# Optimization experiments

Hardware: AMD Instinct MI355X
Metric: run time of the kernel (lower is better)

Reference implementation:

```python
import jax, jax.numpy as jnp
import numpy as np

N_HEADS, N_POINTS, N_LEVELS = 8, 4, 1


def _bilinear(val, x, y):
    """Bilinear sample with zero padding. val: (H, W, D); x, y: (N,) pixel coords.
    Matches torch grid_sample / ms_deform_attn CUDA bilinear (zeros outside)."""
    H, W, _ = val.shape
    x0 = jnp.floor(x)
    y0 = jnp.floor(y)
    dx = (x - x0)[..., None]
    dy = (y - y0)[..., None]
    x0i = x0.astype(jnp.int32)
    y0i = y0.astype(jnp.int32)

    def g(yi, xi):
        inb = ((yi >= 0) & (yi < H) & (xi >= 0) & (xi < W))[..., None]
        yc = jnp.clip(yi, 0, H - 1)
        xc = jnp.clip(xi, 0, W - 1)
        return val[yc, xc] * inb

    v00 = g(y0i, x0i)
    v01 = g(y0i, x0i + 1)
    v10 = g(y0i + 1, x0i)
    v11 = g(y0i + 1, x0i + 1)
    return (v00 * (1 - dx) * (1 - dy) + v01 * dx * (1 - dy)
            + v10 * (1 - dx) * dy + v11 * dx * dy)


def setup_inputs() -> dict:
    key = jax.random.key(0)
    ks = jax.random.split(key, 10)
    V, Lq, C = 5, 4096, 256
    H, W = 128, 240
    nH, P, L = N_HEADS, N_POINTS, N_LEVELS

    query = jax.random.normal(ks[0], (V, Lq, C), jnp.float32)
    reference_points = jax.random.uniform(ks[1], (V, Lq, L, 2), jnp.float32)
    src0 = jax.random.normal(ks[2], (V, C, H, W), jnp.float32)
    camera_ray0 = jax.random.normal(ks[3], (V, H, W, 3), jnp.float32)
    input_spatial_shapes = jnp.array([[H, W]], jnp.int32)
    input_level_start_index = jnp.array([0], jnp.int32)

    # rayconv: Linear(d_model+3 -> d_model), xavier-like
    W_ray = jax.random.normal(ks[4], (C + 3, C), jnp.float32) * (2.0 / (C + 3 + C)) ** 0.5
    b_ray = jnp.zeros((C,), jnp.float32)

    # sampling_offsets: small random weight + the grid bias from _reset_parameters
    W_so = jax.random.normal(ks[5], (C, nH * L * P * 2), jnp.float32) * 0.01
    thetas = np.arange(nH, dtype=np.float64) * (2.0 * np.pi / nH)
    grid = np.stack([np.cos(thetas), np.sin(thetas)], -1)
    grid = grid / np.abs(grid).max(-1, keepdims=True)
    grid = np.tile(grid[:, None, None, :], (1, L, P, 1))  # (nH, L, P, 2)
    grid = grid * (np.arange(P) + 1)[None, None, :, None]
    b_so = jnp.asarray(grid.reshape(-1), jnp.float32)

    W_aw = jax.random.normal(ks[6], (C, nH * L * P), jnp.float32) * 0.01
    b_aw = jnp.zeros((nH * L * P,), jnp.float32)

    W_out = jax.random.normal(ks[7], (C, C), jnp.float32) * (2.0 / (2 * C)) ** 0.5
    b_out = jnp.zeros((C,), jnp.float32)

    return {"query": query, "reference_points": reference_points, "src0": src0,
            "camera_ray0": camera_ray0, "input_spatial_shapes": input_spatial_shapes,
            "input_level_start_index": input_level_start_index,
            "W_ray": W_ray, "b_ray": b_ray, "W_so": W_so, "b_so": b_so,
            "W_aw": W_aw, "b_aw": b_aw, "W_out": W_out, "b_out": b_out}


def reference(query, reference_points, src0, camera_ray0, input_spatial_shapes,
              input_level_start_index, W_ray, b_ray, W_so, b_so, W_aw, b_aw,
              W_out, b_out):
    V, Lq, C = query.shape
    _, _, H, W = src0.shape
    nH, P, L = N_HEADS, N_POINTS, N_LEVELS
    dh = C // nH

    # --- reference-point features via grid_sample (align_corners=False) ---
    g = jnp.clip(reference_points[:, :, 0, :] * 2.0 - 1.0, -1.1, 1.1)  # (V,Lq,2)
    gx = (g[..., 0] + 1.0) * (W * 0.5) - 0.5
    gy = (g[..., 1] + 1.0) * (H * 0.5) - 0.5
    src_hw = jnp.transpose(src0, (0, 2, 3, 1))  # (V,H,W,C)
    ref_feat = jax.vmap(_bilinear)(src_hw, gx, gy)  # (V,Lq,C)

    # --- value = rayconv(concat(flattened features, camera ray embeds)) ---
    src_flat = jnp.transpose(src0.reshape(V, C, H * W), (0, 2, 1))  # (V,Len_in,C)
    cam_flat = camera_ray0.reshape(V, H * W, 3)
    input_flatten = jnp.concatenate([src_flat, cam_flat], -1)  # (V,Len_in,C+3)
    value = input_flatten @ W_ray + b_ray  # (V,Len_in,C)
    # (V,nH,H,W,dh) for per-head bilinear gathering
    value_h = jnp.transpose(value.reshape(V, H, W, nH, dh), (0, 3, 1, 2, 4))

    # --- offsets & attention weights from (ref_feat + query) ---
    feat = ref_feat + query  # (V,Lq,C)  [n_levels==1 so the level dim collapses]
    so = (feat @ W_so + b_so).reshape(V, Lq, nH, L, P, 2)
    aw = jax.nn.softmax((feat @ W_aw + b_aw).reshape(V, Lq, nH, L * P), -1)
    aw = aw.reshape(V, Lq, nH, L, P)

    # normalizer = (W, H)
    norm = jnp.stack([input_spatial_shapes[0, 1],
                      input_spatial_shapes[0, 0]]).astype(query.dtype)
    loc = reference_points[:, :, None, :, None, :] + so / norm  # (V,Lq,nH,L,P,2)

    # --- multi-scale deformable gather (single level) ---
    lx = loc[:, :, :, 0, :, 0]  # (V,Lq,nH,P)
    ly = loc[:, :, :, 0, :, 1]
    x_im = jnp.transpose(lx, (0, 2, 1, 3)).reshape(V, nH, Lq * P) * W - 0.5
    y_im = jnp.transpose(ly, (0, 2, 1, 3)).reshape(V, nH, Lq * P) * H - 0.5
    sampled = jax.vmap(jax.vmap(_bilinear))(value_h, x_im, y_im)  # (V,nH,Lq*P,dh)
    sampled = sampled.reshape(V, nH, Lq, P, dh)

    out = jnp.einsum('vhqpd,vqhp->vqhd', sampled, aw[:, :, :, 0, :])
    out = out.reshape(V, Lq, C)
    return out @ W_out + b_out
```

## Files before the change

kernel.cpp:

```cpp
#include <hip/hip_runtime.h>

#define V_  5
#define LQ  4096
#define C_  256
#define H_  128
#define W_  240
#define HW_ (H_*W_)
#define NH  8
#define DH  32
#define NP  4

typedef __attribute__((ext_vector_type(8))) short bf16x8;
typedef __attribute__((ext_vector_type(4))) float f32x4;

__device__ __forceinline__ unsigned f2b(float f) {
    unsigned u = __float_as_uint(f);
    return (u + 0x7fffu + ((u >> 16) & 1u)) >> 16;
}
__device__ __forceinline__ unsigned pack2(float a, float b) {
    return f2b(a) | (f2b(b) << 16);
}

__global__ __launch_bounds__(256) void k_prep(const float* __restrict__ W_ray,
                                              const float* __restrict__ W_out,
                                              const float* __restrict__ W_so,
                                              const float* __restrict__ W_aw,
                                              unsigned char* __restrict__ imgR,
                                              unsigned char* __restrict__ imgO,
                                              unsigned char* __restrict__ imgF)
{
    int g = blockIdx.x * 256 + threadIdx.x;
    if (g < 16384) {
        int imgid = g >> 13;
        int cid = g & 8191;
        int kt = cid >> 10, rest = cid & 1023;
        int n = rest >> 2, c = rest & 3;
        const float* Wm = imgid ? W_out : W_ray;
        unsigned char* img = imgid ? imgO : imgR;
        int k0 = kt * 32 + c * 8;
        unsigned u0 = pack2(Wm[(size_t)(k0+0)*C_ + n], Wm[(size_t)(k0+1)*C_ + n]);
        unsigned u1 = pack2(Wm[(size_t)(k0+2)*C_ + n], Wm[(size_t)(k0+3)*C_ + n]);
        unsigned u2 = pack2(Wm[(size_t)(k0+4)*C_ + n], Wm[(size_t)(k0+5)*C_ + n]);
        unsigned u3 = pack2(Wm[(size_t)(k0+6)*C_ + n], Wm[(size_t)(k0+7)*C_ + n]);
        *(uint4*)(img + kt*16384 + ((n*64 + c*16) ^ ((n & 7) << 4))) =
            make_uint4(u0, u1, u2, u3);
    } else {
        int f = g - 16384;
        int kt = f / 384;
        int rest = f % 384;
        int n = rest >> 2, c = rest & 3;
        int k0 = kt * 32 + c * 8;
        float w[8];
        #pragma unroll
        for (int e = 0; e < 8; ++e)
            w[e] = (n < 64) ? W_so[(size_t)(k0+e)*64 + n]
                            : W_aw[(size_t)(k0+e)*32 + (n - 64)];
        *(uint4*)(imgF + (size_t)(((kt*96 + n)*4 + c)*16)) =
            make_uint4(pack2(w[0],w[1]), pack2(w[2],w[3]),
                       pack2(w[4],w[5]), pack2(w[6],w[7]));
    }
}

__global__ __launch_bounds__(256) void k_transpose(const float* __restrict__ src,
                                                   unsigned short* __restrict__ dst) {
    __shared__ float tile[32][33];
    int v    = blockIdx.z;
    int pix0 = blockIdx.x * 32;
    int c0   = blockIdx.y * 32;
    int tx = threadIdx.x;
    int ty = threadIdx.y;
    const float* s = src + (size_t)v * C_ * HW_;
    unsigned short* d = dst + (size_t)v * HW_ * C_;
    #pragma unroll
    for (int i = 0; i < 32; i += 8)
        tile[ty + i][tx] = s[(size_t)(c0 + ty + i) * HW_ + pix0 + tx];
    __syncthreads();
    #pragma unroll
    for (int i = 0; i < 32; i += 8)
        d[(size_t)(pix0 + ty + i) * C_ + c0 + tx] = (unsigned short)f2b(tile[tx][ty + i]);
}

__global__ __launch_bounds__(256) void k_feat(
    const float* __restrict__ query, const float* __restrict__ refp,
    const unsigned short* __restrict__ srcT,
    const unsigned char* __restrict__ imgF,
    const float* __restrict__ b_so, const float* __restrict__ b_aw,
    float2* __restrict__ coords, float* __restrict__ aw_out)
{
    __shared__ __align__(16) char feat_b[8][2048];
    __shared__ float so_s[32][66];
    __shared__ float aw_s[32][34];

    int t  = threadIdx.x;
    int wid = t >> 6, lane = t & 63;
    int v  = blockIdx.x >> 7;
    int q0 = (blockIdx.x & 127) << 5;

    {
        int ql = t >> 3, sub = t & 7;
        int q = q0 + ql;
        float rx = refp[((size_t)v*LQ + q)*2 + 0];
        float ry = refp[((size_t)v*LQ + q)*2 + 1];
        float gx = fminf(fmaxf(rx*2.f - 1.f, -1.1f), 1.1f);
        float gy = fminf(fmaxf(ry*2.f - 1.f, -1.1f), 1.1f);
        float x = (gx + 1.f) * (W_ * 0.5f) - 0.5f;
        float y = (gy + 1.f) * (H_ * 0.5f) - 0.5f;
        float xf = floorf(x), yf = floorf(y);
        int x0 = (int)xf, y0 = (int)yf;
        float dx = x - xf, dy = y - yf;
        float wgt[4] = {(1.f-dx)*(1.f-dy), dx*(1.f-dy), (1.f-dx)*dy, dx*dy};
        int xs[4] = {x0, x0+1, x0,   x0+1};
        int ys[4] = {y0, y0,   y0+1, y0+1};

        float accv[32];
        const float* qr = query + ((size_t)v*LQ + q)*C_ + sub*32;
        #pragma unroll
        for (int w2 = 0; w2 < 8; ++w2) {
            float4 qv = *(const float4*)(qr + w2*4);
            accv[w2*4+0]=qv.x; accv[w2*4+1]=qv.y; accv[w2*4+2]=qv.z; accv[w2*4+3]=qv.w;
        }
        #pragma unroll
        for (int cn = 0; cn < 4; ++cn) {
            int xi = xs[cn], yi = ys[cn];
            if (xi >= 0 && xi < W_ && yi >= 0 && yi < H_) {
                float wq = wgt[cn];
                const uint4* cr = (const uint4*)(srcT +
                    ((size_t)v*HW_ + (size_t)yi*W_ + xi)*C_ + sub*32);
                #pragma unroll
                for (int w2 = 0; w2 < 4; ++w2) {
                    uint4 uv = cr[w2];
                    unsigned uu[4] = {uv.x, uv.y, uv.z, uv.w};
                    #pragma unroll
                    for (int p2 = 0; p2 < 4; ++p2) {
                        accv[w2*8 + p2*2 + 0] += wq * __uint_as_float(uu[p2] << 16);
                        accv[w2*8 + p2*2 + 1] += wq * __uint_as_float(uu[p2] & 0xffff0000u);
                    }
                }
            }
        }
        #pragma unroll
        for (int c2 = 0; c2 < 4; ++c2) {
            uint4 w;
            w.x = pack2(accv[c2*8+0], accv[c2*8+1]);
            w.y = pack2(accv[c2*8+2], accv[c2*8+3]);
            w.z = pack2(accv[c2*8+4], accv[c2*8+5]);
            w.w = pack2(accv[c2*8+6], accv[c2*8+7]);
            *(uint4*)(feat_b[sub] + ((ql*64 + c2*16) ^ ((ql & 7) << 4))) = w;
        }
    }
    __syncthreads();

    #pragma unroll
    for (int jj = 0; jj < 3; ++jj) {
        int j  = wid*3 + jj;
        int mi = j / 6, ni = j % 6;
        f32x4 acc = {};
        #pragma unroll
        for (int kt = 0; kt < 8; ++kt) {
            int row = mi*16 + (lane & 15);
            bf16x8 afr = *(const bf16x8*)(feat_b[kt] +
                          ((row*64 + (lane>>4)*16) ^ ((row & 7) << 4)));
            bf16x8 bfr = *(const bf16x8*)(imgF +
                          (size_t)(((kt*96 + ni*16 + (lane & 15))*4 + (lane>>4))*16));
            acc = __builtin_amdgcn_mfma_f32_16x16x32_bf16(afr, bfr, acc, 0, 0, 0);
        }
        int col = ni*16 + (lane & 15);
        float bias = (col < 64) ? b_so[col] : b_aw[col - 64];
        #pragma unroll
        for (int r = 0; r < 4; ++r) {
            int row = mi*16 + (lane>>4)*4 + r;
            float vv = acc[r] + bias;
            if (col < 64) so_s[row][col] = vv;
            else          aw_s[row][col - 64] = vv;
        }
    }
    __syncthreads();

    {
        int jq = t >> 3, h = t & 7;
        int qq = q0 + jq;
        float rx = refp[((size_t)v*LQ + qq)*2 + 0];
        float ry = refp[((size_t)v*LQ + qq)*2 + 1];
        float sc[4], m = -1e30f;
        #pragma unroll
        for (int p = 0; p < 4; ++p) { sc[p] = aw_s[jq][h*4+p]; m = fmaxf(m, sc[p]); }
        float den = 0.f;
        #pragma unroll
        for (int p = 0; p < 4; ++p) { sc[p] = __expf(sc[p]-m); den += sc[p]; }
        float inv = 1.f/den;
        size_t base = ((size_t)v*LQ + qq)*(NH*NP) + h*NP;
        #pragma unroll
        for (int p = 0; p < 4; ++p) {
            aw_out[base + p] = sc[p]*inv;
            float sx = so_s[jq][h*8 + p*2 + 0];
            float sy = so_s[jq][h*8 + p*2 + 1];
            coords[base + p] = make_float2(rx*W_ + sx - 0.5f, ry*H_ + sy - 0.5f);
        }
    }
}

__global__ __launch_bounds__(256, 3) void k_value(
    const float* __restrict__ src0, const float* __restrict__ cam,
    const float* __restrict__ W_ray, const float* __restrict__ b_ray,
    const unsigned char* __restrict__ imgB,
    unsigned short* __restrict__ value)
{
    __shared__ __align__(16) char As[2][4096];
    __shared__ __align__(16) char Bs[2][16384];

    int t = threadIdx.x;
    int wid = t >> 6, lane = t & 63;
    int mtile = blockIdx.x;
    int v   = mtile / 480;
    int pl0 = (mtile % 480) * 64;
    const float* A = src0 + (size_t)v * C_ * HW_;

    int sm = t & 63, skg = t >> 6;
    const float* aptr = A + (size_t)(skg*8)*HW_ + pl0 + sm;
    const uint4* bptr = (const uint4*)imgB + t*4;

    f32x4 acc[4][4] = {};
    float ar[8]; uint4 br[4];

    #pragma unroll
    for (int j = 0; j < 8; ++j) ar[j] = aptr[(size_t)j*HW_];
    #pragma unroll
    for (int j = 0; j < 4; ++j) br[j] = bptr[j];
    {
        uint4 w; w.x=pack2(ar[0],ar[1]); w.y=pack2(ar[2],ar[3]);
                 w.z=pack2(ar[4],ar[5]); w.w=pack2(ar[6],ar[7]);
        *(uint4*)(As[0] + ((sm*64 + skg*16) ^ ((sm & 7) << 4))) = w;
        #pragma unroll
        for (int j = 0; j < 4; ++j) *(uint4*)(Bs[0] + t*64 + j*16) = br[j];
    }
    __syncthreads();

    int nb = wid * 64;
    for (int kt = 0; kt < 8; ++kt) {
        int cur = kt & 1;
        if (kt < 7) {
            const float* ap = aptr + (size_t)((kt+1)*32)*HW_;
            #pragma unroll
            for (int j = 0; j < 8; ++j) ar[j] = ap[(size_t)j*HW_];
            const uint4* bp = bptr + (kt+1)*1024;
            #pragma unroll
            for (int j = 0; j < 4; ++j) br[j] = bp[j];
        }
        bf16x8 af[4], bf[4];
        #pragma unroll
        for (int i = 0; i < 4; ++i) {
            int m = i*16 + (lane & 15);
            af[i] = *(const bf16x8*)(As[cur] + ((m*64 + (lane>>4)*16) ^ ((m & 7) << 4)));
        }
        #pragma unroll
        for (int j = 0; j < 4; ++j) {
            int n = nb + j*16 + (lane & 15);
            bf[j] = *(const bf16x8*)(Bs[cur] + ((n*64 + (lane>>4)*16) ^ ((n & 7) << 4)));
        }
        #pragma unroll
        for (int i = 0; i < 4; ++i)
            #pragma unroll
            for (int j = 0; j < 4; ++j)
                acc[i][j] = __builtin_amdgcn_mfma_f32_16x16x32_bf16(
                                af[i], bf[j], acc[i][j], 0, 0, 0);
        if (kt < 7) {
            uint4 w; w.x=pack2(ar[0],ar[1]); w.y=pack2(ar[2],ar[3]);
                     w.z=pack2(ar[4],ar[5]); w.w=pack2(ar[6],ar[7]);
            *(uint4*)(As[cur^1] + ((sm*64 + skg*16) ^ ((sm & 7) << 4))) = w;
            #pragma unroll
            for (int j = 0; j < 4; ++j) *(uint4*)(Bs[cur^1] + t*64 + j*16) = br[j];
        }
        __syncthreads();
    }

    float wr0[4], wr1[4], wr2[4], bb[4];
    #pragma unroll
    for (int j = 0; j < 4; ++j) {
        int col = nb + j*16 + (lane & 15);
        wr0[j] = W_ray[(size_t)256*C_ + col];
        wr1[j] = W_ray[(size_t)257*C_ + col];
        wr2[j] = W_ray[(size_t)258*C_ + col];
        bb[j]  = b_ray[col];
    }
    #pragma unroll
    for (int i = 0; i < 4; ++i) {
        #pragma unroll
        for (int r = 0; r < 4; ++r) {
            int ml = i*16 + (lane>>4)*4 + r;
            int pix = pl0 + ml;
            const float* cp = cam + ((size_t)v*HW_ + pix)*3;
            float c0v = cp[0], c1v = cp[1], c2v = cp[2];
            size_t rowbase = ((size_t)mtile*64 + ml) * C_;
            #pragma unroll
            for (int j = 0; j < 4; ++j) {
                float o = acc[i][j][r] + bb[j]
                        + c0v*wr0[j] + c1v*wr1[j] + c2v*wr2[j];
                value[rowbase + nb + j*16 + (lane & 15)] = (unsigned short)f2b(o);
            }
        }
    }
}

__global__ __launch_bounds__(256) void k_sample(
    const unsigned short* __restrict__ value, const float2* __restrict__ coords,
    const float* __restrict__ aw, unsigned short* __restrict__ attnb)
{
    int t = threadIdx.x;
    int h = t >> 5;
    int d = t & 31;
    int vq0 = blockIdx.x * 4;
    #pragma unroll
    for (int ql = 0; ql < 4; ++ql) {
        int vq = vq0 + ql;
        int v = vq >> 12;
        size_t cbase = (size_t)vq * (NH*NP) + h*NP;
        const unsigned short* vb = value + (size_t)v*HW_*C_ + h*DH + d;
        float o = 0.f;
        #pragma unroll
        for (int p = 0; p < 4; ++p) {
            float2 cc = coords[cbase + p];
            float a   = aw[cbase + p];
            float xf = floorf(cc.x), yf = floorf(cc.y);
            int x0 = (int)xf, y0 = (int)yf;
            float dx = cc.x - xf, dy = cc.y - yf;
            bool xv0 = (x0 >= 0) & (x0 < W_);
            bool xv1 = (x0 >= -1) & (x0 < W_-1);
            bool yv0 = (y0 >= 0) & (y0 < H_);
            bool yv1 = (y0 >= -1) & (y0 < H_-1);
            float s = 0.f;
            if (yv0 & xv0) s += (1.f-dx)*(1.f-dy) *
                __uint_as_float((unsigned)vb[(size_t)(y0*W_ + x0)*C_] << 16);
            if (yv0 & xv1) s += dx*(1.f-dy) *
                __uint_as_float((unsigned)vb[(size_t)(y0*W_ + x0+1)*C_] << 16);
            if (yv1 & xv0) s += (1.f-dx)*dy *
                __uint_as_float((unsigned)vb[(size_t)((y0+1)*W_ + x0)*C_] << 16);
            if (yv1 & xv1) s += dx*dy *
                __uint_as_float((unsigned)vb[(size_t)((y0+1)*W_ + x0+1)*C_] << 16);
            o += a * s;
        }
        attnb[(size_t)vq*C_ + h*DH + d] = (unsigned short)f2b(o);
    }
}

__global__ __launch_bounds__(256, 3) void k_out(
    const unsigned short* __restrict__ attnb, const unsigned char* __restrict__ imgB,
    const float* __restrict__ b_out, float* __restrict__ outp)
{
    __shared__ __align__(16) char As[2][4096];
    __shared__ __align__(16) char Bs[2][16384];

    int t = threadIdx.x;
    int wid = t >> 6, lane = t & 63;
    int m0 = blockIdx.x * 64;

    int sm = t >> 2, skg = t & 3;
    const uint4* bptr = (const uint4*)imgB + t*4;

    f32x4 acc[4][4] = {};
    uint4 ar, br[4];

    ar = *(const uint4*)(attnb + (size_t)(m0+sm)*C_ + skg*8);
    #pragma unroll
    for (int j = 0; j < 4; ++j) br[j] = bptr[j];
    *(uint4*)(As[0] + ((sm*64 + skg*16) ^ ((sm & 7) << 4))) = ar;
    #pragma unroll
    for (int j = 0; j < 4; ++j) *(uint4*)(Bs[0] + t*64 + j*16) = br[j];
    __syncthreads();

    int nb = wid * 64;
    for (int kt = 0; kt < 8; ++kt) {
        int cur = kt & 1;
        if (kt < 7) {
            ar = *(const uint4*)(attnb + (size_t)(m0+sm)*C_ + (kt+1)*32 + skg*8);
            const uint4* bp = bptr + (kt+1)*1024;
            #pragma unroll
            for (int j = 0; j < 4; ++j) br[j] = bp[j];
        }
        bf16x8 af[4], bf[4];
        #pragma unroll
        for (int i = 0; i < 4; ++i) {
            int m = i*16 + (lane & 15);
            af[i] = *(const bf16x8*)(As[cur] + ((m*64 + (lane>>4)*16) ^ ((m & 7) << 4)));
        }
        #pragma unroll
        for (int j = 0; j < 4; ++j) {
            int n = nb + j*16 + (lane & 15);
            bf[j] = *(const bf16x8*)(Bs[cur] + ((n*64 + (lane>>4)*16) ^ ((n & 7) << 4)));
        }
        #pragma unroll
        for (int i = 0; i < 4; ++i)
            #pragma unroll
            for (int j = 0; j < 4; ++j)
                acc[i][j] = __builtin_amdgcn_mfma_f32_16x16x32_bf16(
                                af[i], bf[j], acc[i][j], 0, 0, 0);
        if (kt < 7) {
            *(uint4*)(As[cur^1] + ((sm*64 + skg*16) ^ ((sm & 7) << 4))) = ar;
            #pragma unroll
            for (int j = 0; j < 4; ++j) *(uint4*)(Bs[cur^1] + t*64 + j*16) = br[j];
        }
        __syncthreads();
    }

    float bb[4];
    #pragma unroll
    for (int j = 0; j < 4; ++j) bb[j] = b_out[nb + j*16 + (lane & 15)];
    #pragma unroll
    for (int i = 0; i < 4; ++i) {
        #pragma unroll
        for (int r = 0; r < 4; ++r) {
            int ml = i*16 + (lane>>4)*4 + r;
            size_t rowbase = (size_t)(m0 + ml) * C_;
            #pragma unroll
            for (int j = 0; j < 4; ++j)
                outp[rowbase + nb + j*16 + (lane & 15)] = acc[i][j][r] + bb[j];
        }
    }
}

extern "C" void kernel_launch(void* const* d_in, const int* in_sizes, int n_in,
                              void* d_out, int out_size, void* d_ws, size_t ws_size,
                              hipStream_t stream)
{
    (void)in_sizes; (void)n_in; (void)out_size; (void)ws_size;
    const float* query = (const float*)d_in[0];
    const float* refp  = (const float*)d_in[1];
    const float* src0  = (const float*)d_in[2];
    const float* cam   = (const float*)d_in[3];
    const float* W_ray = (const float*)d_in[6];
    const float* b_ray = (const float*)d_in[7];
    const float* W_so  = (const float*)d_in[8];
    const float* b_so  = (const float*)d_in[9];
    const float* W_aw  = (const float*)d_in[10];
    const float* b_aw  = (const float*)d_in[11];
    const float* W_out = (const float*)d_in[12];
    const float* b_out = (const float*)d_in[13];
    float* out = (float*)d_out;

    char* ws = (char*)d_ws;
    unsigned short* buf0  = (unsigned short*)(ws);
    unsigned char*  imgR  = (unsigned char*)(ws + 78643200);
    unsigned char*  imgO  = (unsigned char*)(ws + 78774272);
    unsigned char*  imgF  = (unsigned char*)(ws + 78905344);
    float2*         coords= (float2*)(ws + 78954496);
    float*          awbuf = (float*)(ws + 84197376);
    unsigned short* attnb = (unsigned short*)(ws + 86818816);

    k_prep<<<dim3(76), 256, 0, stream>>>(W_ray, W_out, W_so, W_aw, imgR, imgO, imgF);
    k_transpose<<<dim3(HW_/32, C_/32, V_), dim3(32,8), 0, stream>>>(src0, buf0);
    k_feat<<<dim3(V_*(LQ/32)), 256, 0, stream>>>(query, refp, buf0, imgF,
                                                 b_so, b_aw, coords, awbuf);
    k_value<<<dim3((V_*HW_)/64), 256, 0, stream>>>(src0, cam, W_ray, b_ray, imgR, buf0);
    k_sample<<<dim3(V_*LQ/4), 256, 0, stream>>>(buf0, coords, awbuf, attnb);
    k_out<<<dim3(V_*LQ/64), 256, 0, stream>>>(attnb, imgO, b_out, out);
}
```

Baseline: 447.2 us.

## Fuse src transpose into value GEMM by writing bf16 tiles from shared memory

Removes the separate transpose kernel. The value GEMM kernel now also writes the bf16 A tile it already staged in shared memory out to a new srcT buffer, which k_feat reads instead. This saves one full read of src0 (about 157 MB of fp32) and one kernel launch. In exchange k_value does extra global stores, the workspace grows by a second bf16 buffer, and k_value now has to run before k_feat.

New measurement: 429.1 us. 4.1% less time.

```diff
diff --git a/kernel.cpp b/kernel.cpp
--- a/kernel.cpp
+++ b/kernel.cpp
@@ -61,23 +61,113 @@
     }
 }
 
-__global__ __launch_bounds__(256) void k_transpose(const float* __restrict__ src,
-                                                   unsigned short* __restrict__ dst) {
-    __shared__ float tile[32][33];
-    int v    = blockIdx.z;
-    int pix0 = blockIdx.x * 32;
-    int c0   = blockIdx.y * 32;
-    int tx = threadIdx.x;
-    int ty = threadIdx.y;
-    const float* s = src + (size_t)v * C_ * HW_;
-    unsigned short* d = dst + (size_t)v * HW_ * C_;
-    #pragma unroll
-    for (int i = 0; i < 32; i += 8)
-        tile[ty + i][tx] = s[(size_t)(c0 + ty + i) * HW_ + pix0 + tx];
+__global__ __launch_bounds__(256, 3) void k_value(
+    const float* __restrict__ src0, const float* __restrict__ cam,
+    const float* __restrict__ W_ray, const float* __restrict__ b_ray,
+    const unsigned char* __restrict__ imgB,
+    unsigned short* __restrict__ value,
+    unsigned short* __restrict__ srcT)
+{
+    __shared__ __align__(16) char As[2][4096];
+    __shared__ __align__(16) char Bs[2][16384];
+
+    int t = threadIdx.x;
+    int wid = t >> 6, lane = t & 63;
+    int mtile = blockIdx.x;
+    int v   = mtile / 480;
+    int pl0 = (mtile % 480) * 64;
+    const float* A = src0 + (size_t)v * C_ * HW_;
+
+    int sm = t & 63, skg = t >> 6;
+    const float* aptr = A + (size_t)(skg*8)*HW_ + pl0 + sm;
+    const uint4* bptr = (const uint4*)imgB + t*4;
+
+    int tp  = t >> 2, tc = t & 3;
+
+    f32x4 acc[4][4] = {};
+    float ar[8]; uint4 br[4];
+
+    #pragma unroll
+    for (int j = 0; j < 8; ++j) ar[j] = aptr[(size_t)j*HW_];
+    #pragma unroll
+    for (int j = 0; j < 4; ++j) br[j] = bptr[j];
+    {
+        uint4 w; w.x=pack2(ar[0],ar[1]); w.y=pack2(ar[2],ar[3]);
+                 w.z=pack2(ar[4],ar[5]); w.w=pack2(ar[6],ar[7]);
+        *(uint4*)(As[0] + ((sm*64 + skg*16) ^ ((sm & 7) << 4))) = w;
+        #pragma unroll
+        for (int j = 0; j < 4; ++j) *(uint4*)(Bs[0] + t*64 + j*16) = br[j];
+    }
     __syncthreads();
-    #pragma unroll
-    for (int i = 0; i < 32; i += 8)
-        d[(size_t)(pix0 + ty + i) * C_ + c0 + tx] = (unsigned short)f2b(tile[tx][ty + i]);
+
+    int nb = wid * 64;
+    for (int kt = 0; kt < 8; ++kt) {
+        int cur = kt & 1;
+        if (kt < 7) {
+            const float* ap = aptr + (size_t)((kt+1)*32)*HW_;
+            #pragma unroll
+            for (int j = 0; j < 8; ++j) ar[j] = ap[(size_t)j*HW_];
+            const uint4* bp = bptr + (kt+1)*1024;
+            #pragma unroll
+            for (int j = 0; j < 4; ++j) br[j] = bp[j];
+        }
+        bf16x8 af[4], bf[4];
+        #pragma unroll
+        for (int i = 0; i < 4; ++i) {
+            int m = i*16 + (lane & 15);
+            af[i] = *(const bf16x8*)(As[cur] + ((m*64 + (lane>>4)*16) ^ ((m & 7) << 4)));
+        }
+        #pragma unroll
+        for (int j = 0; j < 4; ++j) {
+            int n = nb + j*16 + (lane & 15);
+            bf[j] = *(const bf16x8*)(Bs[cur] + ((n*64 + (lane>>4)*16) ^ ((n & 7) << 4)));
+        }
+        {
+            uint4 row = *(const uint4*)(As[cur] + ((tp*64 + tc*16) ^ ((tp & 7) << 4)));
+            *(uint4*)(srcT + ((size_t)(mtile*64 + tp))*C_ + kt*32 + tc*8) = row;
+        }
+        #pragma unroll
+        for (int i = 0; i < 4; ++i)
+            #pragma unroll
+            for (int j = 0; j < 4; ++j)
+                acc[i][j] = __builtin_amdgcn_mfma_f32_16x16x32_bf16(
+                                af[i], bf[j], acc[i][j], 0, 0, 0);
+        if (kt < 7) {
+            uint4 w; w.x=pack2(ar[0],ar[1]); w.y=pack2(ar[2],ar[3]);
+                     w.z=pack2(ar[4],ar[5]); w.w=pack2(ar[6],ar[7]);
+            *(uint4*)(As[cur^1] + ((sm*64 + skg*16) ^ ((sm & 7) << 4))) = w;
+            #pragma unroll
+            for (int j = 0; j < 4; ++j) *(uint4*)(Bs[cur^1] + t*64 + j*16) = br[j];
+        }
+        __syncthreads();
+    }
+
+    float wr0[4], wr1[4], wr2[4], bb[4];
+    #pragma unroll
+    for (int j = 0; j < 4; ++j) {
+        int col = nb + j*16 + (lane & 15);
+        wr0[j] = W_ray[(size_t)256*C_ + col];
+        wr1[j] = W_ray[(size_t)257*C_ + col];
+        wr2[j] = W_ray[(size_t)258*C_ + col];
+        bb[j]  = b_ray[col];
+    }
+    #pragma unroll
+    for (int i = 0; i < 4; ++i) {
+        #pragma unroll
+        for (int r = 0; r < 4; ++r) {
+            int ml = i*16 + (lane>>4)*4 + r;
+            int pix = pl0 + ml;
+            const float* cp = cam + ((size_t)v*HW_ + pix)*3;
+            float c0v = cp[0], c1v = cp[1], c2v = cp[2];
+            size_t rowbase = ((size_t)mtile*64 + ml) * C_;
+            #pragma unroll
+            for (int j = 0; j < 4; ++j) {
+                float o = acc[i][j][r] + bb[j]
+                        + c0v*wr0[j] + c1v*wr1[j] + c2v*wr2[j];
+                value[rowbase + nb + j*16 + (lane & 15)] = (unsigned short)f2b(o);
+            }
+        }
+    }
 }
 
 __global__ __launch_bounds__(256) void k_feat(
@@ -195,108 +285,6 @@
             float sx = so_s[jq][h*8 + p*2 + 0];
             float sy = so_s[jq][h*8 + p*2 + 1];
             coords[base + p] = make_float2(rx*W_ + sx - 0.5f, ry*H_ + sy - 0.5f);
-        }
-    }
-}
-
-__global__ __launch_bounds__(256, 3) void k_value(
-    const float* __restrict__ src0, const float* __restrict__ cam,
-    const float* __restrict__ W_ray, const float* __restrict__ b_ray,
-    const unsigned char* __restrict__ imgB,
-    unsigned short* __restrict__ value)
-{
-    __shared__ __align__(16) char As[2][4096];
-    __shared__ __align__(16) char Bs[2][16384];
-
-    int t = threadIdx.x;
-    int wid = t >> 6, lane = t & 63;
-    int mtile = blockIdx.x;
-    int v   = mtile / 480;
-    int pl0 = (mtile % 480) * 64;
-    const float* A = src0 + (size_t)v * C_ * HW_;
-
-    int sm = t & 63, skg = t >> 6;
-    const float* aptr = A + (size_t)(skg*8)*HW_ + pl0 + sm;
-    const uint4* bptr = (const uint4*)imgB + t*4;
-
-    f32x4 acc[4][4] = {};
-    float ar[8]; uint4 br[4];
-
-    #pragma unroll
-    for (int j = 0; j < 8; ++j) ar[j] = aptr[(size_t)j*HW_];
-    #pragma unroll
-    for (int j = 0; j < 4; ++j) br[j] = bptr[j];
-    {
-        uint4 w; w.x=pack2(ar[0],ar[1]); w.y=pack2(ar[2],ar[3]);
-                 w.z=pack2(ar[4],ar[5]); w.w=pack2(ar[6],ar[7]);
-        *(uint4*)(As[0] + ((sm*64 + skg*16) ^ ((sm & 7) << 4))) = w;
-        #pragma unroll
-        for (int j = 0; j < 4; ++j) *(uint4*)(Bs[0] + t*64 + j*16) = br[j];
-    }
-    __syncthreads();
-
-    int nb = wid * 64;
-    for (int kt = 0; kt < 8; ++kt) {
-        int cur = kt & 1;
-        if (kt < 7) {
-            const float* ap = aptr + (size_t)((kt+1)*32)*HW_;
-            #pragma unroll
-            for (int j = 0; j < 8; ++j) ar[j] = ap[(size_t)j*HW_];
-            const uint4* bp = bptr + (kt+1)*1024;
-            #pragma unroll
-            for (int j = 0; j < 4; ++j) br[j] = bp[j];
-        }
-        bf16x8 af[4], bf[4];
-        #pragma unroll
-        for (int i = 0; i < 4; ++i) {
-            int m = i*16 + (lane & 15);
-            af[i] = *(const bf16x8*)(As[cur] + ((m*64 + (lane>>4)*16) ^ ((m & 7) << 4)));
-        }
-        #pragma unroll
-        for (int j = 0; j < 4; ++j) {
-            int n = nb + j*16 + (lane & 15);
-            bf[j] = *(const bf16x8*)(Bs[cur] + ((n*64 + (lane>>4)*16) ^ ((n & 7) << 4)));
-        }
-        #pragma unroll
-        for (int i = 0; i < 4; ++i)
-            #pragma unroll
-            for (int j = 0; j < 4; ++j)
-                acc[i][j] = __builtin_amdgcn_mfma_f32_16x16x32_bf16(
-                                af[i], bf[j], acc[i][j], 0, 0, 0);
-        if (kt < 7) {
-            uint4 w; w.x=pack2(ar[0],ar[1]); w.y=pack2(ar[2],ar[3]);
-                     w.z=pack2(ar[4],ar[5]); w.w=pack2(ar[6],ar[7]);
-            *(uint4*)(As[cur^1] + ((sm*64 + skg*16) ^ ((sm & 7) << 4))) = w;
-            #pragma unroll
-            for (int j = 0; j < 4; ++j) *(uint4*)(Bs[cur^1] + t*64 + j*16) = br[j];
-        }
-        __syncthreads();
-    }
-
-    float wr0[4], wr1[4], wr2[4], bb[4];
-    #pragma unroll
-    for (int j = 0; j < 4; ++j) {
-        int col = nb + j*16 + (lane & 15);
-        wr0[j] = W_ray[(size_t)256*C_ + col];
-        wr1[j] = W_ray[(size_t)257*C_ + col];
-        wr2[j] = W_ray[(size_t)258*C_ + col];
-        bb[j]  = b_ray[col];
-    }
-    #pragma unroll
-    for (int i = 0; i < 4; ++i) {
-        #pragma unroll
-        for (int r = 0; r < 4; ++r) {
-            int ml = i*16 + (lane>>4)*4 + r;
-            int pix = pl0 + ml;
-            const float* cp = cam + ((size_t)v*HW_ + pix)*3;
-            float c0v = cp[0], c1v = cp[1], c2v = cp[2];
-            size_t rowbase = ((size_t)mtile*64 + ml) * C_;
-            #pragma unroll
-            for (int j = 0; j < 4; ++j) {
-                float o = acc[i][j][r] + bb[j]
-                        + c0v*wr0[j] + c1v*wr1[j] + c2v*wr2[j];
-                value[rowbase + nb + j*16 + (lane & 15)] = (unsigned short)f2b(o);
-            }
         }
     }
 }
@@ -437,19 +425,20 @@
     float* out = (float*)d_out;
 
     char* ws = (char*)d_ws;
-    unsigned short* buf0  = (unsigned short*)(ws);
-    unsigned char*  imgR  = (unsigned char*)(ws + 78643200);
-    unsigned char*  imgO  = (unsigned char*)(ws + 78774272);
-    unsigned char*  imgF  = (unsigned char*)(ws + 78905344);
-    float2*         coords= (float2*)(ws + 78954496);
-    float*          awbuf = (float*)(ws + 84197376);
-    unsigned short* attnb = (unsigned short*)(ws + 86818816);
+    unsigned short* value = (unsigned short*)(ws);
+    unsigned short* srcT  = (unsigned short*)(ws + 78643200);
+    unsigned char*  imgR  = (unsigned char*)(ws + 157286400);
+    unsigned char*  imgO  = (unsigned char*)(ws + 157417472);
+    unsigned char*  imgF  = (unsigned char*)(ws + 157548544);
+    float2*         coords= (float2*)(ws + 157597696);
+    float*          awbuf = (float*)(ws + 162840576);
+    unsigned short* attnb = (unsigned short*)(ws + 165462016);
 
     k_prep<<<dim3(76), 256, 0, stream>>>(W_ray, W_out, W_so, W_aw, imgR, imgO, imgF);
-    k_transpose<<<dim3(HW_/32, C_/32, V_), dim3(32,8), 0, stream>>>(src0, buf0);
-    k_feat<<<dim3(V_*(LQ/32)), 256, 0, stream>>>(query, refp, buf0, imgF,
+    k_value<<<dim3((V_*HW_)/64), 256, 0, stream>>>(src0, cam, W_ray, b_ray, imgR,
+                                                   value, srcT);
+    k_feat<<<dim3(V_*(LQ/32)), 256, 0, stream>>>(query, refp, srcT, imgF,
                                                  b_so, b_aw, coords, awbuf);
-    k_value<<<dim3((V_*HW_)/64), 256, 0, stream>>>(src0, cam, W_ray, b_ray, imgR, buf0);
-    k_sample<<<dim3(V_*LQ/4), 256, 0, stream>>>(buf0, coords, awbuf, attnb);
+    k_sample<<<dim3(V_*LQ/4), 256, 0, stream>>>(value, coords, awbuf, attnb);
     k_out<<<dim3(V_*LQ/64), 256, 0, stream>>>(attnb, imgO, b_out, out);
 }
```
